# Optimization experiments

Measured on AMD Instinct MI355X. Metric: run time of the kernel, lower is better.

Reference implementation:

```python
import jax, jax.numpy as jnp
import numpy as np

DIM = 256
MUL = 4
NUM_ENTRIES = 64
B, K = 16, 64
R = MUL * DIM


def setup_inputs() -> dict:
    key = jax.random.key(0)
    k_slots, k_idx, k_w1, k_w2 = jax.random.split(key, 4)
    slots = jax.random.normal(k_slots, (B, K, DIM), dtype=jnp.float32)
    indices = jax.random.randint(k_idx, (B, K), 0, NUM_ENTRIES, dtype=jnp.int64)
    # xavier_normal: std = sqrt(2 / (fan_in + fan_out)) over last two dims
    std1 = float(np.sqrt(2.0 / (DIM + R)))
    std2 = float(np.sqrt(2.0 / (R + DIM)))
    w1 = jax.random.normal(k_w1, (NUM_ENTRIES, DIM, R), dtype=jnp.float32) * std1
    w2 = jax.random.normal(k_w2, (NUM_ENTRIES, R, DIM), dtype=jnp.float32) * std2
    b1 = jnp.zeros((NUM_ENTRIES, R), dtype=jnp.float32)
    b2 = jnp.zeros((NUM_ENTRIES, DIM), dtype=jnp.float32)
    return {"slots": slots, "w1": w1, "b1": b1, "w2": w2, "b2": b2, "indices": indices}


def reference(slots, w1, b1, w2, b2, indices):
    # gather per-(b,k) expert weights, then 2-layer MLP (matvec per slot)
    h = jnp.einsum('bkd,bkdr->bkr', slots, w1[indices]) + b1[indices]  # (B,K,R)
    h = jax.nn.relu(h)
    out = jnp.einsum('bkr,bkrd->bkd', h, w2[indices]) + b2[indices]    # (B,K,DIM)
    return out
```

## Files before the change

kernel.cpp:

```cpp
#include <hip/hip_runtime.h>
#include <stdint.h>

#define DIMC 256
#define RTOT 1024
#define NE 64
#define NSLOT 1024
#define RCN 8
#define RCW 128
#define TILE 32
#define XSTR 264
#define NT 16

typedef short bfrag __attribute__((ext_vector_type(8)));
typedef float f32x4 __attribute__((ext_vector_type(4)));

#define VMCNT(N) asm volatile("s_waitcnt vmcnt(" #N ")" ::: "memory")
#define LGKM0_BAR()                                          \
  do {                                                       \
    asm volatile("s_waitcnt lgkmcnt(0)" ::: "memory");       \
    __builtin_amdgcn_s_barrier();                            \
  } while (0)

static __device__ __forceinline__ unsigned short f2bf(float f) {
  unsigned u = __float_as_uint(f);
  return (unsigned short)((u + 0x7FFFu + ((u >> 16) & 1u)) >> 16);
}

static __device__ __forceinline__ bfrag pack8(const float* f) {
  union { unsigned short u[8]; bfrag v; } r;
#pragma unroll
  for (int i = 0; i < 8; ++i) r.u[i] = f2bf(f[i]);
  return r.v;
}

static __device__ __forceinline__ void gload16(const float* g, float* l) {
  __builtin_amdgcn_global_load_lds(
      (const __attribute__((address_space(1))) void*)g,
      (__attribute__((address_space(3))) void*)l, 16, 0, 0);
}

__global__ __launch_bounds__(512, 4) void mlp_kernel(
    const float* __restrict__ slots, const float* __restrict__ w1,
    const float* __restrict__ b1, const float* __restrict__ w2,
    const float* __restrict__ b2, const int* __restrict__ indices,
    float* __restrict__ out) {
  const int e  = blockIdx.x;
  const int rc = blockIdx.y;
  const int t  = threadIdx.x;
  const int l  = t & 63;
  const int w  = t >> 6;
  const int ln = l & 15;
  const int kg = l >> 4;
  const int rbase = rc * RCW;

  __shared__ __align__(16) float WT[3][4096];
  __shared__ __align__(16) unsigned short X[TILE * XSTR];
  __shared__ unsigned short blist[NSLOT];
  __shared__ int sid[TILE];
  __shared__ int bn_s;

  if (t == 0) bn_s = 0;
  __syncthreads();
  {
    int i0 = indices[t] & (NE - 1);
    int i1 = indices[t + 512] & (NE - 1);
    if (i0 == e) { int p = atomicAdd(&bn_s, 1); blist[p] = (unsigned short)t; }
    if (i1 == e) { int p = atomicAdd(&bn_s, 1); blist[p] = (unsigned short)(t + 512); }
  }
  __syncthreads();
  const int n = bn_s;
  if (n == 0) return;

  const float* w1e = w1 + (size_t)e * DIMC * RTOT + rbase;
  const float* w2e = w2 + (size_t)e * RTOT * DIMC + (size_t)rbase * DIMC;
  const int   c    = w * 16 + ln;
  const float b1v  = b1[e * RTOT + rbase + c];

  auto STAGE = [&](int tt, float* buf) {
    if (tt < 8) {
      const float* g = w1e + (size_t)(tt * 32 + (t >> 5)) * RTOT + (t & 31) * 4;
      gload16(g, buf + t * 4);
      gload16(g + (size_t)16 * RTOT, buf + 2048 + t * 4);
    } else {
      const int rt = (tt - 8) >> 1, dh = tt & 1;
      const float* g =
          w2e + (size_t)(rt * 32 + (t >> 5)) * DIMC + dh * 128 + (t & 31) * 4;
      gload16(g, buf + t * 4);
      gload16(g + 16 * DIMC, buf + 2048 + t * 4);
    }
  };

  for (int s0 = 0; s0 < n; s0 += TILE) {
    const int m = (n - s0 < TILE) ? (n - s0) : TILE;

    LGKM0_BAR();
    if (t < TILE) sid[t] = (t < m) ? (int)blist[s0 + t] : 0;
    LGKM0_BAR();

#pragma unroll
    for (int i = t; i < TILE * 64; i += 512) {
      int s = i >> 6, d4 = (i & 63) * 4;
      float4 v = make_float4(0.f, 0.f, 0.f, 0.f);
      if (s < m) v = ((const float4*)slots)[(size_t)sid[s] * 64 + (i & 63)];
      union { unsigned short u[4]; uint2 q; } p;
      p.u[0] = f2bf(v.x); p.u[1] = f2bf(v.y);
      p.u[2] = f2bf(v.z); p.u[3] = f2bf(v.w);
      *(uint2*)&X[s * XSTR + d4] = p.q;
    }

    f32x4 acc1[2];
    acc1[0] = (f32x4)(0.f); acc1[1] = (f32x4)(0.f);
    f32x4 acc2[2][2];
#pragma unroll
    for (int mt = 0; mt < 2; ++mt)
#pragma unroll
      for (int dh = 0; dh < 2; ++dh) acc2[mt][dh] = (f32x4)(0.f);

    STAGE(0, WT[0]);
    STAGE(1, WT[1]);

#pragma unroll
    for (int tt = 0; tt < NT; ++tt) {
      if (tt < NT - 1) VMCNT(2);
      else             VMCNT(0);
      LGKM0_BAR();

      if (tt == 8) {
#pragma unroll
        for (int mt = 0; mt < 2; ++mt)
#pragma unroll
          for (int reg = 0; reg < 4; ++reg) {
            float h = fmaxf(acc1[mt][reg] + b1v, 0.f);
            X[(mt * 16 + kg * 4 + reg) * XSTR + c] = f2bf(h);
          }
        LGKM0_BAR();
      }

      if (tt + 2 < NT) STAGE(tt + 2, WT[(tt + 2) % 3]);

      {
        const float* buf = WT[tt % 3];
        float f[8];
#pragma unroll
        for (int j = 0; j < 8; ++j) f[j] = buf[(kg * 8 + j) * RCW + c];
        bfrag b = pack8(f);
        if (tt < 8) {
          bfrag a0 = *(const bfrag*)&X[ln * XSTR + tt * 32 + kg * 8];
          bfrag a1 = *(const bfrag*)&X[(16 + ln) * XSTR + tt * 32 + kg * 8];
          acc1[0] = __builtin_amdgcn_mfma_f32_16x16x32_bf16(a0, b, acc1[0], 0, 0, 0);
          acc1[1] = __builtin_amdgcn_mfma_f32_16x16x32_bf16(a1, b, acc1[1], 0, 0, 0);
        } else {
          const int rt = (tt - 8) >> 1, dh = tt & 1;
          bfrag a0 = *(const bfrag*)&X[ln * XSTR + rt * 32 + kg * 8];
          bfrag a1 = *(const bfrag*)&X[(16 + ln) * XSTR + rt * 32 + kg * 8];
          acc2[0][dh] = __builtin_amdgcn_mfma_f32_16x16x32_bf16(a0, b, acc2[0][dh], 0, 0, 0);
          acc2[1][dh] = __builtin_amdgcn_mfma_f32_16x16x32_bf16(a1, b, acc2[1][dh], 0, 0, 0);
        }
      }
    }

#pragma unroll
    for (int dh = 0; dh < 2; ++dh) {
      const int col = dh * 128 + c;
      const float b2v = (rc == 0) ? b2[e * DIMC + col] : 0.f;
#pragma unroll
      for (int mt = 0; mt < 2; ++mt)
#pragma unroll
        for (int reg = 0; reg < 4; ++reg) {
          const int row = mt * 16 + kg * 4 + reg;
          if (row < m)
            atomicAdd(&out[(size_t)sid[row] * DIMC + col],
                      acc2[mt][dh][reg] + b2v);
        }
    }
  }
}

extern "C" void kernel_launch(void* const* d_in, const int* in_sizes, int n_in,
                              void* d_out, int out_size, void* d_ws, size_t ws_size,
                              hipStream_t stream) {
  const float* slots   = (const float*)d_in[0];
  const float* w1      = (const float*)d_in[1];
  const float* b1      = (const float*)d_in[2];
  const float* w2      = (const float*)d_in[3];
  const float* b2      = (const float*)d_in[4];
  const int*   indices = (const int*)d_in[5];
  float* out = (float*)d_out;

  (void)d_ws; (void)ws_size;

  hipMemsetAsync(d_out, 0, (size_t)out_size * sizeof(float), stream);
  mlp_kernel<<<dim3(NE, RCN), 512, 0, stream>>>(slots, w1, b1, w2, b2,
                                                indices, out);
}
```

Baseline: 170.4 us.

## Replace output atomics with per-chunk partial buffers and a reduction kernel

Each of the eight R-chunk blocks now writes its partial second-layer result into its own workspace slice instead of atomically adding into the output. A separate reduce kernel then sums the eight slices and adds the b2 bias for each slot. This removes the memset and the float atomic contention. In exchange it adds an extra launch and about 8 MB of workspace writes and reads. If the workspace is too small, the code falls back to the atomic path.

```diff
diff --git a/kernel.cpp b/kernel.cpp
--- a/kernel.cpp
+++ b/kernel.cpp
@@ -39,11 +39,12 @@
       (__attribute__((address_space(3))) void*)l, 16, 0, 0);
 }
 
+template <int USE_WS>
 __global__ __launch_bounds__(512, 4) void mlp_kernel(
     const float* __restrict__ slots, const float* __restrict__ w1,
     const float* __restrict__ b1, const float* __restrict__ w2,
     const float* __restrict__ b2, const int* __restrict__ indices,
-    float* __restrict__ out) {
+    float* __restrict__ part, float* __restrict__ out) {
   const int e  = blockIdx.x;
   const int rc = blockIdx.y;
   const int t  = threadIdx.x;
@@ -75,6 +76,7 @@
   const float* w2e = w2 + (size_t)e * RTOT * DIMC + (size_t)rbase * DIMC;
   const int   c    = w * 16 + ln;
   const float b1v  = b1[e * RTOT + rbase + c];
+  float* prc = part + (size_t)rc * NSLOT * DIMC;
 
   auto STAGE = [&](int tt, float* buf) {
     if (tt < 8) {
@@ -162,18 +164,37 @@
 #pragma unroll
     for (int dh = 0; dh < 2; ++dh) {
       const int col = dh * 128 + c;
-      const float b2v = (rc == 0) ? b2[e * DIMC + col] : 0.f;
+      const float b2v =
+          (!USE_WS && rc == 0) ? b2[e * DIMC + col] : 0.f;
 #pragma unroll
       for (int mt = 0; mt < 2; ++mt)
 #pragma unroll
         for (int reg = 0; reg < 4; ++reg) {
           const int row = mt * 16 + kg * 4 + reg;
-          if (row < m)
-            atomicAdd(&out[(size_t)sid[row] * DIMC + col],
-                      acc2[mt][dh][reg] + b2v);
+          if (row < m) {
+            if (USE_WS) {
+              prc[(size_t)sid[row] * DIMC + col] = acc2[mt][dh][reg];
+            } else {
+              atomicAdd(&out[(size_t)sid[row] * DIMC + col],
+                        acc2[mt][dh][reg] + b2v);
+            }
+          }
         }
     }
   }
+}
+
+__global__ __launch_bounds__(256) void reduce_kernel(
+    const float* __restrict__ part, const float* __restrict__ b2,
+    const int* __restrict__ indices, float* __restrict__ out) {
+  const int i = blockIdx.x * 256 + threadIdx.x;
+  const int slot = i >> 6;
+  const int e = indices[slot] & (NE - 1);
+  f32x4 s = *(const f32x4*)(b2 + e * DIMC + (i & 63) * 4);
+#pragma unroll
+  for (int rc = 0; rc < RCN; ++rc)
+    s += *(const f32x4*)(part + (size_t)rc * NSLOT * DIMC + (size_t)i * 4);
+  *(f32x4*)(out + (size_t)i * 4) = s;
 }
 
 extern "C" void kernel_launch(void* const* d_in, const int* in_sizes, int n_in,
@@ -187,9 +208,16 @@
   const int*   indices = (const int*)d_in[5];
   float* out = (float*)d_out;
 
-  (void)d_ws; (void)ws_size;
-
-  hipMemsetAsync(d_out, 0, (size_t)out_size * sizeof(float), stream);
-  mlp_kernel<<<dim3(NE, RCN), 512, 0, stream>>>(slots, w1, b1, w2, b2,
-                                                indices, out);
-}
+  const size_t need = (size_t)RCN * NSLOT * DIMC * sizeof(float);
+  if (ws_size >= need) {
+    float* part = (float*)d_ws;
+    mlp_kernel<1><<<dim3(NE, RCN), 512, 0, stream>>>(slots, w1, b1, w2, b2,
+                                                     indices, part, out);
+    reduce_kernel<<<NSLOT * DIMC / 4 / 256, 256, 0, stream>>>(part, b2,
+                                                              indices, out);
+  } else {
+    hipMemsetAsync(d_out, 0, (size_t)out_size * sizeof(float), stream);
+    mlp_kernel<0><<<dim3(NE, RCN), 512, 0, stream>>>(slots, w1, b1, w2, b2,
+                                                     indices, nullptr, out);
+  }
+}
```

New measurement: 163.2 us. -4.2%, faster.

## Per-wave private weight staging and workspace split-K reduction replacing atomics

Applied to the files above, without the earlier changes.

Each wave now stages its own weight slice into a private LDS triple buffer, so the per-stage block barriers are gone and waves only wait on their own vmcnt. The second GEMM is re-tiled so each wave owns 32 output columns. When workspace is large enough, partial results go to a per-rc scratch buffer instead of global atomicAdd. The last block per expert, detected through a done counter, sums the partials and adds b2. This costs extra global traffic for the partials and a serialized final reduction in one block per expert, and it depends on the harness providing about 8 MB of workspace.

```diff
diff --git a/kernel.cpp b/kernel.cpp
--- a/kernel.cpp
+++ b/kernel.cpp
@@ -9,15 +9,15 @@
 #define RCW 128
 #define TILE 32
 #define XSTR 264
-#define NT 16
 
 typedef short bfrag __attribute__((ext_vector_type(8)));
 typedef float f32x4 __attribute__((ext_vector_type(4)));
 
-#define VMCNT(N) asm volatile("s_waitcnt vmcnt(" #N ")" ::: "memory")
+#define WAITV(n) asm volatile("s_waitcnt vmcnt(" #n ")" ::: "memory")
+#define LGKM0()  asm volatile("s_waitcnt lgkmcnt(0)" ::: "memory")
 #define LGKM0_BAR()                                          \
   do {                                                       \
-    asm volatile("s_waitcnt lgkmcnt(0)" ::: "memory");       \
+    LGKM0();                                                 \
     __builtin_amdgcn_s_barrier();                            \
   } while (0)
 
@@ -39,10 +39,12 @@
       (__attribute__((address_space(3))) void*)l, 16, 0, 0);
 }
 
+template <int USE_WS>
 __global__ __launch_bounds__(512, 4) void mlp_kernel(
     const float* __restrict__ slots, const float* __restrict__ w1,
     const float* __restrict__ b1, const float* __restrict__ w2,
     const float* __restrict__ b2, const int* __restrict__ indices,
+    float* __restrict__ part, int* __restrict__ done,
     float* __restrict__ out) {
   const int e  = blockIdx.x;
   const int rc = blockIdx.y;
@@ -53,11 +55,12 @@
   const int kg = l >> 4;
   const int rbase = rc * RCW;
 
-  __shared__ __align__(16) float WT[3][4096];
+  __shared__ __align__(16) float WB[8][1536];
   __shared__ __align__(16) unsigned short X[TILE * XSTR];
   __shared__ unsigned short blist[NSLOT];
   __shared__ int sid[TILE];
   __shared__ int bn_s;
+  __shared__ int lastf;
 
   if (t == 0) bn_s = 0;
   __syncthreads();
@@ -75,27 +78,30 @@
   const float* w2e = w2 + (size_t)e * RTOT * DIMC + (size_t)rbase * DIMC;
   const int   c    = w * 16 + ln;
   const float b1v  = b1[e * RTOT + rbase + c];
-
-  auto STAGE = [&](int tt, float* buf) {
-    if (tt < 8) {
-      const float* g = w1e + (size_t)(tt * 32 + (t >> 5)) * RTOT + (t & 31) * 4;
-      gload16(g, buf + t * 4);
-      gload16(g + (size_t)16 * RTOT, buf + 2048 + t * 4);
-    } else {
-      const int rt = (tt - 8) >> 1, dh = tt & 1;
-      const float* g =
-          w2e + (size_t)(rt * 32 + (t >> 5)) * DIMC + dh * 128 + (t & 31) * 4;
-      gload16(g, buf + t * 4);
-      gload16(g + 16 * DIMC, buf + 2048 + t * 4);
-    }
+  float* WBw = WB[w];
+  float* prc = part + (size_t)rc * NSLOT * DIMC;
+
+  auto STG1 = [&](int g) {
+#pragma unroll
+    for (int q = 0; q < 2; ++q)
+      gload16(w1e + (size_t)(g * 32 + q * 16 + (l >> 2)) * RTOT +
+                  w * 16 + (l & 3) * 4,
+              WBw + (g % 3) * 512 + q * 256 + l * 4);
+  };
+  auto STG2 = [&](int u) {
+#pragma unroll
+    for (int q = 0; q < 2; ++q)
+      gload16(w2e + (size_t)(u * 16 + q * 8 + (l >> 3)) * DIMC +
+                  w * 32 + (l & 7) * 4,
+              WBw + (u % 3) * 512 + q * 256 + l * 4);
   };
 
   for (int s0 = 0; s0 < n; s0 += TILE) {
     const int m = (n - s0 < TILE) ? (n - s0) : TILE;
 
-    LGKM0_BAR();
+    __syncthreads();
     if (t < TILE) sid[t] = (t < m) ? (int)blist[s0 + t] : 0;
-    LGKM0_BAR();
+    __syncthreads();
 
 #pragma unroll
     for (int i = t; i < TILE * 64; i += 512) {
@@ -107,71 +113,114 @@
       p.u[2] = f2bf(v.z); p.u[3] = f2bf(v.w);
       *(uint2*)&X[s * XSTR + d4] = p.q;
     }
+    __syncthreads();
 
     f32x4 acc1[2];
     acc1[0] = (f32x4)(0.f); acc1[1] = (f32x4)(0.f);
+    STG1(0); STG1(1); STG1(2);
+
+#define CONS1(ks)                                                           \
+  {                                                                         \
+    const float* base = WBw + ((ks) % 3) * 512;                             \
+    float f[8];                                                             \
+    _Pragma("unroll") for (int j = 0; j < 8; ++j)                           \
+        f[j] = base[(kg * 8 + j) * 16 + ln];                                \
+    bfrag b = pack8(f);                                                     \
+    bfrag a0 = *(const bfrag*)&X[ln * XSTR + (ks) * 32 + kg * 8];           \
+    bfrag a1 = *(const bfrag*)&X[(16 + ln) * XSTR + (ks) * 32 + kg * 8];    \
+    acc1[0] = __builtin_amdgcn_mfma_f32_16x16x32_bf16(a0, b, acc1[0], 0, 0, 0); \
+    acc1[1] = __builtin_amdgcn_mfma_f32_16x16x32_bf16(a1, b, acc1[1], 0, 0, 0); \
+  }
+
+    WAITV(4); CONS1(0); LGKM0(); STG1(3);
+    WAITV(4); CONS1(1); LGKM0(); STG1(4);
+    WAITV(4); CONS1(2); LGKM0(); STG1(5);
+    WAITV(4); CONS1(3); LGKM0(); STG1(6);
+    WAITV(4); CONS1(4); LGKM0(); STG1(7);
+    WAITV(4); CONS1(5);
+    WAITV(2); CONS1(6);
+    WAITV(0); CONS1(7);
+#undef CONS1
+
+    LGKM0();
+    STG2(0); STG2(1); STG2(2);
+
+    LGKM0_BAR();
+
+#pragma unroll
+    for (int mt = 0; mt < 2; ++mt)
+#pragma unroll
+      for (int reg = 0; reg < 4; ++reg) {
+        float h = fmaxf(acc1[mt][reg] + b1v, 0.f);
+        X[(mt * 16 + kg * 4 + reg) * XSTR + c] = f2bf(h);
+      }
+    LGKM0_BAR();
+
     f32x4 acc2[2][2];
 #pragma unroll
     for (int mt = 0; mt < 2; ++mt)
 #pragma unroll
-      for (int dh = 0; dh < 2; ++dh) acc2[mt][dh] = (f32x4)(0.f);
-
-    STAGE(0, WT[0]);
-    STAGE(1, WT[1]);
-
-#pragma unroll
-    for (int tt = 0; tt < NT; ++tt) {
-      if (tt < NT - 1) VMCNT(2);
-      else             VMCNT(0);
-      LGKM0_BAR();
-
-      if (tt == 8) {
-#pragma unroll
-        for (int mt = 0; mt < 2; ++mt)
-#pragma unroll
-          for (int reg = 0; reg < 4; ++reg) {
-            float h = fmaxf(acc1[mt][reg] + b1v, 0.f);
-            X[(mt * 16 + kg * 4 + reg) * XSTR + c] = f2bf(h);
-          }
-        LGKM0_BAR();
-      }
-
-      if (tt + 2 < NT) STAGE(tt + 2, WT[(tt + 2) % 3]);
-
-      {
-        const float* buf = WT[tt % 3];
-        float f[8];
-#pragma unroll
-        for (int j = 0; j < 8; ++j) f[j] = buf[(kg * 8 + j) * RCW + c];
-        bfrag b = pack8(f);
-        if (tt < 8) {
-          bfrag a0 = *(const bfrag*)&X[ln * XSTR + tt * 32 + kg * 8];
-          bfrag a1 = *(const bfrag*)&X[(16 + ln) * XSTR + tt * 32 + kg * 8];
-          acc1[0] = __builtin_amdgcn_mfma_f32_16x16x32_bf16(a0, b, acc1[0], 0, 0, 0);
-          acc1[1] = __builtin_amdgcn_mfma_f32_16x16x32_bf16(a1, b, acc1[1], 0, 0, 0);
-        } else {
-          const int rt = (tt - 8) >> 1, dh = tt & 1;
-          bfrag a0 = *(const bfrag*)&X[ln * XSTR + rt * 32 + kg * 8];
-          bfrag a1 = *(const bfrag*)&X[(16 + ln) * XSTR + rt * 32 + kg * 8];
-          acc2[0][dh] = __builtin_amdgcn_mfma_f32_16x16x32_bf16(a0, b, acc2[0][dh], 0, 0, 0);
-          acc2[1][dh] = __builtin_amdgcn_mfma_f32_16x16x32_bf16(a1, b, acc2[1][dh], 0, 0, 0);
-        }
-      }
-    }
-
-#pragma unroll
-    for (int dh = 0; dh < 2; ++dh) {
-      const int col = dh * 128 + c;
-      const float b2v = (rc == 0) ? b2[e * DIMC + col] : 0.f;
+      for (int nt = 0; nt < 2; ++nt) acc2[mt][nt] = (f32x4)(0.f);
+
+#define CONS2(rt)                                                           \
+  {                                                                         \
+    const float* base = WBw + ((rt * 2 + (kg >> 1)) % 3) * 512 +            \
+                        (kg & 1) * 256 + ln;                                \
+    bfrag a0 = *(const bfrag*)&X[ln * XSTR + (rt) * 32 + kg * 8];           \
+    bfrag a1 = *(const bfrag*)&X[(16 + ln) * XSTR + (rt) * 32 + kg * 8];    \
+    _Pragma("unroll") for (int nt = 0; nt < 2; ++nt) {                      \
+      float f[8];                                                           \
+      _Pragma("unroll") for (int j = 0; j < 8; ++j)                         \
+          f[j] = base[j * 32 + nt * 16];                                    \
+      bfrag b = pack8(f);                                                   \
+      acc2[0][nt] = __builtin_amdgcn_mfma_f32_16x16x32_bf16(a0, b, acc2[0][nt], 0, 0, 0); \
+      acc2[1][nt] = __builtin_amdgcn_mfma_f32_16x16x32_bf16(a1, b, acc2[1][nt], 0, 0, 0); \
+    }                                                                       \
+  }
+
+    WAITV(2); CONS2(0); LGKM0(); STG2(3); STG2(4);
+    WAITV(2); CONS2(1); LGKM0(); STG2(5); STG2(6);
+    WAITV(2); CONS2(2); LGKM0(); STG2(7);
+    WAITV(0); CONS2(3);
+#undef CONS2
+
+#pragma unroll
+    for (int nt = 0; nt < 2; ++nt) {
+      const int col = w * 32 + nt * 16 + ln;
+      const float b2v = (!USE_WS && rc == 0) ? b2[e * DIMC + col] : 0.f;
 #pragma unroll
       for (int mt = 0; mt < 2; ++mt)
 #pragma unroll
         for (int reg = 0; reg < 4; ++reg) {
           const int row = mt * 16 + kg * 4 + reg;
-          if (row < m)
-            atomicAdd(&out[(size_t)sid[row] * DIMC + col],
-                      acc2[mt][dh][reg] + b2v);
+          if (row < m) {
+            if (USE_WS) {
+              prc[(size_t)sid[row] * DIMC + col] = acc2[mt][nt][reg];
+            } else {
+              atomicAdd(&out[(size_t)sid[row] * DIMC + col],
+                        acc2[mt][nt][reg] + b2v);
+            }
+          }
         }
+    }
+  }
+
+  if (USE_WS) {
+    __threadfence();
+    if (t == 0) lastf = (atomicAdd(&done[e], 1) == RCN - 1);
+    __syncthreads();
+    if (lastf) {
+      __threadfence();
+      for (int i = t; i < n * 64; i += 512) {
+        const int s  = blist[i >> 6];
+        const int c4 = i & 63;
+        f32x4 acc = *(const f32x4*)(b2 + e * DIMC + c4 * 4);
+#pragma unroll
+        for (int r2 = 0; r2 < RCN; ++r2)
+          acc += *(const f32x4*)(part + (size_t)r2 * NSLOT * DIMC +
+                                 (size_t)s * DIMC + c4 * 4);
+        *(f32x4*)(out + (size_t)s * DIMC + c4 * 4) = acc;
+      }
     }
   }
 }
@@ -187,9 +236,18 @@
   const int*   indices = (const int*)d_in[5];
   float* out = (float*)d_out;
 
-  (void)d_ws; (void)ws_size;
-
-  hipMemsetAsync(d_out, 0, (size_t)out_size * sizeof(float), stream);
-  mlp_kernel<<<dim3(NE, RCN), 512, 0, stream>>>(slots, w1, b1, w2, b2,
-                                                indices, out);
-}
+  const size_t part_bytes = (size_t)RCN * NSLOT * DIMC * sizeof(float);
+  const size_t need = part_bytes + 256;
+  if (ws_size >= need) {
+    float* part = (float*)d_ws;
+    int*   done = (int*)((char*)d_ws + part_bytes);
+    hipMemsetAsync(done, 0, NE * sizeof(int), stream);
+    mlp_kernel<1><<<dim3(NE, RCN), 512, 0, stream>>>(slots, w1, b1, w2, b2,
+                                                     indices, part, done, out);
+  } else {
+    hipMemsetAsync(d_out, 0, (size_t)out_size * sizeof(float), stream);
+    mlp_kernel<0><<<dim3(NE, RCN), 512, 0, stream>>>(slots, w1, b1, w2, b2,
+                                                     indices, nullptr, nullptr,
+                                                     out);
+  }
+}
```

Result: slower. 344.3 us (+102.1%).
